# Performance work log

Hardware: AMD Instinct MI355X
Metric: run time of the kernel (lower is better)

## Reference

```python
import jax, jax.numpy as jnp
import numpy as np

DEPTH = 24; D_MODEL = 192; D_INNER = 384; D_STATE = 16; DT_RANK = 12; D_CONV = 4
H = 32; W = 3200; P = 16; NP = (W // P) * (H // P)  # 400 patches
NCLS = 22; BATCH = 4; EPS = 1e-5


def _rmsnorm(x, w):
    return x * jax.lax.rsqrt(jnp.mean(x * x, axis=-1, keepdims=True) + EPS) * w


def _causal_dwconv(x, w, b):
    # x: (B, L, D), w: (D, K) depthwise, left-padded causal conv (mamba conv1d)
    D = x.shape[-1]; K = w.shape[-1]
    xp = jnp.pad(jnp.swapaxes(x, 1, 2), ((0, 0), (0, 0), (K - 1, 0)))
    y = jax.lax.conv_general_dilated(xp, w[:, None, :], (1,), 'VALID',
            dimension_numbers=('NCH', 'OIH', 'NCH'), feature_group_count=D)
    return jnp.swapaxes(y + b[None, :, None], 1, 2)


def _selective_scan(x, dt, Bm, Cm, A, Dsk):
    # x, dt: (B, L, d); Bm, Cm: (B, L, n); A: (d, n); Dsk: (d,)
    dA = jnp.exp(dt[..., None] * A)                  # (B, L, d, n)
    dBx = (dt * x)[..., None] * Bm[:, :, None, :]    # (B, L, d, n)
    h0 = jnp.zeros((x.shape[0], x.shape[2], A.shape[1]), x.dtype)

    def step(h, inp):
        a, bx, c = inp
        h = a * h + bx
        return h, jnp.einsum('bdn,bn->bd', h, c)

    _, ys = jax.lax.scan(step, h0,
        (jnp.swapaxes(dA, 0, 1), jnp.swapaxes(dBx, 0, 1), jnp.swapaxes(Cm, 0, 1)))
    return jnp.swapaxes(ys, 0, 1) + x * Dsk


def _mamba_dir(xz, cw_l, cb_l, xpw, dtw, dtb, A, Dsk):
    xx, z = jnp.split(xz, 2, axis=-1)
    xx = jax.nn.silu(_causal_dwconv(xx, cw_l, cb_l))
    dbl = xx @ xpw.T                                  # (B, L, dt_rank + 2n)
    dt = jax.nn.softplus(dbl[..., :DT_RANK] @ dtw.T + dtb)
    Bm = dbl[..., DT_RANK:DT_RANK + D_STATE]
    Cm = dbl[..., DT_RANK + D_STATE:]
    y = _selective_scan(xx, dt, Bm, Cm, A, Dsk)
    return y * jax.nn.silu(z)


def _forward(x, pe_w, pe_b, cls_token, pos_embed, norm_w, in_proj_w, cw, cb,
             xproj_w, dtproj_w, dtproj_b, A_log, A_b_log, Dp, outproj_w,
             norm_f_w, head_w, head_b):
    B = x.shape[0]
    # patch embed: conv2d stride=kernel=16 on (B,1,H,W)
    y = jax.lax.conv_general_dilated(x[:, None], pe_w, (P, P), 'VALID',
            dimension_numbers=('NCHW', 'OIHW', 'NCHW')) + pe_b[None, :, None, None]
    tok = jnp.transpose(y, (0, 2, 3, 1)).reshape(B, -1, D_MODEL)   # (B, NP, D)
    tok = jnp.concatenate([jnp.broadcast_to(cls_token, (B, 1, D_MODEL)), tok], axis=1)
    tok = tok + pos_embed

    def layer_step(carry, p):
        hidden, residual = carry
        nw, ipw, cw_l, cb_l, xpw, dtw, dtb, Al, Abl, Dsk, opw = p
        residual = residual + hidden          # fused add (residual_in_fp32: all fp32)
        h = _rmsnorm(residual, nw)
        xz = h @ ipw.T                         # (B, L, 2*d_inner)
        y_f = _mamba_dir(xz, cw_l, cb_l, xpw, dtw, dtb, -jnp.exp(Al), Dsk)
        y_b = _mamba_dir(xz[:, ::-1], cw_l, cb_l, xpw, dtw, dtb, -jnp.exp(Abl), Dsk)[:, ::-1]
        return ((y_f + y_b) @ opw.T, residual), None

    # NOTE: source sets residual = x AND hidden = x before the loop, so the
    (hidden, residual), _ = jax.lax.scan(
        layer_step, (tok, tok),
        (norm_w, in_proj_w, cw, cb, xproj_w, dtproj_w, dtproj_b, A_log, A_b_log, Dp, outproj_w))
    out = _rmsnorm(residual + hidden, norm_f_w)
    return out[:, 0] @ head_w.T + head_b          # (B, n_classes)


def setup_inputs() -> dict:
    key = jax.random.key(0)
    ks = jax.random.split(key, 12)

    def n(k, shape, scale):
        return jax.random.normal(k, shape, jnp.float32) * scale

    a_init = jnp.tile(jnp.log(jnp.arange(1, D_STATE + 1, dtype=jnp.float32))[None, None, :],
                      (DEPTH, D_INNER, 1))
    return {
        'x': n(ks[0], (BATCH, H, W), 1.0),
        'pe_w': n(ks[1], (D_MODEL, 1, P, P), 1.0 / P),
        'pe_b': jnp.zeros((D_MODEL,), jnp.float32),
        'cls_token': n(ks[2], (1, 1, D_MODEL), 0.02),
        'pos_embed': n(ks[3], (1, NP + 1, D_MODEL), 0.02),
        'norm_w': jnp.ones((DEPTH, D_MODEL), jnp.float32),
        'in_proj_w': n(ks[4], (DEPTH, 2 * D_INNER, D_MODEL), D_MODEL ** -0.5),
        'cw': n(ks[5], (DEPTH, D_INNER, D_CONV), D_CONV ** -0.5),
        'cb': jnp.zeros((DEPTH, D_INNER), jnp.float32),
        'xproj_w': n(ks[6], (DEPTH, DT_RANK + 2 * D_STATE, D_INNER), D_INNER ** -0.5),
        'dtproj_w': n(ks[7], (DEPTH, D_INNER, DT_RANK), DT_RANK ** -0.5),
        'dtproj_b': n(ks[8], (DEPTH, D_INNER), 0.1),
        'A_log': a_init,
        'A_b_log': a_init,
        'Dp': jnp.ones((DEPTH, D_INNER), jnp.float32),
        'outproj_w': n(ks[9], (DEPTH, D_MODEL, D_INNER), D_INNER ** -0.5 / np.sqrt(DEPTH)),
        'norm_f_w': jnp.ones((D_MODEL,), jnp.float32),
        'head_w': n(ks[10], (NCLS, D_MODEL), D_MODEL ** -0.5),
        'head_b': jnp.zeros((NCLS,), jnp.float32),
    }


def reference(x, pe_w, pe_b, cls_token, pos_embed, norm_w, in_proj_w, cw, cb,
              xproj_w, dtproj_w, dtproj_b, A_log, A_b_log, Dp, outproj_w,
              norm_f_w, head_w, head_b):
    return _forward(x, pe_w, pe_b, cls_token, pos_embed, norm_w, in_proj_w, cw, cb,
                    xproj_w, dtproj_w, dtproj_b, A_log, A_b_log, Dp, outproj_w,
                    norm_f_w, head_w, head_b)
```

## Files before the change

kernel.cpp:

```cpp
#include <hip/hip_runtime.h>
#include <hip/hip_bf16.h>

#define DEPTH 24
#define DM 192
#define DI 384
#define DS 16
#define DR 12
#define LSEQ 401
#define BATCH 4
#define NTOK (BATCH*LSEQ)
#define NCLS 22
#define NC 16
#define TCH 26

__device__ __forceinline__ float silu_f(float x) { return x / (1.f + __expf(-x)); }

__global__ void patch_embed_k(const float* __restrict__ x,
                              const float* __restrict__ pe_w,
                              const float* __restrict__ pe_b,
                              const float* __restrict__ cls,
                              const float* __restrict__ pos,
                              float* __restrict__ residual, float* __restrict__ hidden)
{
    __shared__ float xp[4][256];
    int g0 = blockIdx.x * 4;
    int c = threadIdx.x;
    #pragma unroll
    for (int j = 0; j < 4; j++) {
        int g = g0 + j;
        int b = g / LSEQ, t = g % LSEQ;
        if (t != 0) {
            int p = t - 1, pi = p / 200, pj = p % 200;
            for (int i = c; i < 256; i += 192) {
                int pp = i >> 4, qq = i & 15;
                xp[j][i] = x[((size_t)(b * 32 + pi * 16 + pp)) * 3200 + pj * 16 + qq];
            }
        }
    }
    __syncthreads();
    float acc[4] = {0.f, 0.f, 0.f, 0.f};
    for (int k = 0; k < 256; k++) {
        float w = pe_w[c * 256 + k];
        #pragma unroll
        for (int j = 0; j < 4; j++) acc[j] += xp[j][k] * w;
    }
    #pragma unroll
    for (int j = 0; j < 4; j++) {
        int g = g0 + j;
        int t = g % LSEQ;
        float v = (t == 0) ? cls[c] : (acc[j] + pe_b[c]);
        v += pos[t * DM + c];
        residual[(size_t)g * DM + c] = v;
        hidden[(size_t)g * DM + c] = v;
    }
}

__global__ __launch_bounds__(256) void gemm_xz_k(
    const float* __restrict__ resin, const float* __restrict__ hidden,
    float* __restrict__ resout, const float* __restrict__ nw,
    const float* __restrict__ ipw, float* __restrict__ xz,
    float* __restrict__ dbl)
{
    __shared__ float As[48][68];
    __shared__ float Ws[48][68];
    __shared__ float srms[64];
    __shared__ float ps[64][4];
    int tid = threadIdx.x;
    for (int i = (blockIdx.y * 12 + blockIdx.x) * 256 + tid; i < 2 * NTOK * 44; i += 312 * 256)
        dbl[i] = 0.f;
    int bn = blockIdx.x * 64;
    int bm = blockIdx.y * 64;
    int rr = tid >> 2, q = tid & 3;
    int m = bm + rr;
    float rv[4][12];
    float s = 0.f;
    if (m < NTOK) {
        const float* rp = resin + (size_t)m * DM;
        const float* hp = hidden + (size_t)m * DM;
        #pragma unroll
        for (int c = 0; c < 4; c++) {
            int base = c * 48 + q * 12;
            #pragma unroll
            for (int i = 0; i < 12; i += 4) {
                float4 a = *(const float4*)&rp[base + i];
                float4 b = *(const float4*)&hp[base + i];
                float r0 = a.x + b.x, r1 = a.y + b.y, r2 = a.z + b.z, r3 = a.w + b.w;
                rv[c][i] = r0; rv[c][i + 1] = r1; rv[c][i + 2] = r2; rv[c][i + 3] = r3;
                s += r0 * r0 + r1 * r1 + r2 * r2 + r3 * r3;
            }
        }
        if (bn == 0) {
            float* op = resout + (size_t)m * DM;
            #pragma unroll
            for (int c = 0; c < 4; c++) {
                int base = c * 48 + q * 12;
                #pragma unroll
                for (int i = 0; i < 12; i += 4)
                    *(float4*)&op[base + i] =
                        make_float4(rv[c][i], rv[c][i + 1], rv[c][i + 2], rv[c][i + 3]);
            }
        }
    } else {
        #pragma unroll
        for (int c = 0; c < 4; c++)
            #pragma unroll
            for (int i = 0; i < 12; i++) rv[c][i] = 0.f;
    }
    ps[rr][q] = s;
    __syncthreads();
    if (q == 0) {
        float tot = ps[rr][0] + ps[rr][1] + ps[rr][2] + ps[rr][3];
        srms[rr] = rsqrtf(tot * (1.f / (float)DM) + 1e-5f);
    }
    __syncthreads();

    int orow = (tid >> 4) * 4;
    int ocol = (tid & 15) * 4;
    int sk = q * 12;
    float acc[4][4] = {};
    for (int c = 0; c < 4; c++) {
        float rs = srms[rr];
        #pragma unroll
        for (int i = 0; i < 12; i++)
            As[sk + i][rr] = rv[c][i] * rs * nw[c * 48 + sk + i];
        const float* wp = ipw + (size_t)(bn + rr) * DM + c * 48 + sk;
        #pragma unroll
        for (int i = 0; i < 12; i++)
            Ws[sk + i][rr] = wp[i];
        __syncthreads();
        #pragma unroll
        for (int kk = 0; kk < 48; kk++) {
            float4 a = *(const float4*)&As[kk][orow];
            float4 w = *(const float4*)&Ws[kk][ocol];
            acc[0][0] += a.x * w.x; acc[0][1] += a.x * w.y; acc[0][2] += a.x * w.z; acc[0][3] += a.x * w.w;
            acc[1][0] += a.y * w.x; acc[1][1] += a.y * w.y; acc[1][2] += a.y * w.z; acc[1][3] += a.y * w.w;
            acc[2][0] += a.z * w.x; acc[2][1] += a.z * w.y; acc[2][2] += a.z * w.z; acc[2][3] += a.z * w.w;
            acc[3][0] += a.w * w.x; acc[3][1] += a.w * w.y; acc[3][2] += a.w * w.z; acc[3][3] += a.w * w.w;
        }
        __syncthreads();
    }
    #pragma unroll
    for (int i = 0; i < 4; i++) {
        int mm = bm + orow + i;
        if (mm >= NTOK) continue;
        *(float4*)&xz[(size_t)mm * (2 * DI) + bn + ocol] =
            make_float4(acc[i][0], acc[i][1], acc[i][2], acc[i][3]);
    }
}

__global__ __launch_bounds__(256) void xproj_conv_k(
    const float* __restrict__ xz,
    const float* __restrict__ cw, const float* __restrict__ cb,
    const float* __restrict__ xpw, float* __restrict__ dbl)
{
    __shared__ float As[96][33];
    __shared__ float Ws[96][48];
    int tid = threadIdx.x;
    int kbase = blockIdx.x * 96;
    int bm = blockIdx.y * 32;
    for (int idx = tid; idx < 96 * 32; idx += 256) {
        int k = idx >> 5, row = idx & 31;
        int m = bm + row;
        float v = 0.f;
        if (m < 2 * NTOK) {
            int dir = m / NTOK;
            int r = m - dir * NTOK;
            int b = r / LSEQ, t = r % LSEQ;
            int ch = kbase + k;
            float a = cb[ch];
            #pragma unroll
            for (int j = 0; j < 4; j++) {
                int tt = t - 3 + j;
                if (tt >= 0) {
                    int st = dir ? (LSEQ - 1 - tt) : tt;
                    a += cw[ch * 4 + j] * xz[((size_t)(b * LSEQ + st)) * (2 * DI) + ch];
                }
            }
            v = silu_f(a);
        }
        As[k][row] = v;
    }
    for (int i = tid; i < 96 * 48; i += 256) {
        int k = i / 48, rr = i % 48;
        Ws[k][rr] = (rr < 44) ? xpw[(size_t)rr * DI + kbase + k] : 0.f;
    }
    __syncthreads();
    int row = tid & 31, cg = tid >> 5;
    int cbase = cg * 6;
    float acc[6] = {};
    #pragma unroll 4
    for (int kk = 0; kk < 96; kk++) {
        float a = As[kk][row];
        #pragma unroll
        for (int j = 0; j < 6; j++) acc[j] += a * Ws[kk][cbase + j];
    }
    int m = bm + row;
    if (m < 2 * NTOK) {
        #pragma unroll
        for (int j = 0; j < 6; j++) {
            int cc = cbase + j;
            if (cc < 44) atomicAdd(&dbl[(size_t)m * 44 + cc], acc[j]);
        }
    }
}

__global__ __launch_bounds__(256) void scan_part_k(
    const float* __restrict__ xz, const float* __restrict__ dbl,
    const float* __restrict__ cw, const float* __restrict__ cb,
    const float* __restrict__ dtw, const float* __restrict__ dtb,
    const float* __restrict__ A_log, const float* __restrict__ A_b_log,
    float* __restrict__ hloc, float* __restrict__ Pc)
{
    __shared__ float sdbl[TCH][28];
    __shared__ float sdt[TCH][16];
    __shared__ float sxx[TCH][16];
    __shared__ float sw[16][12];
    __shared__ float sb2[16];
    int dblk = blockIdx.x, chunk = blockIdx.y;
    int db = blockIdx.z;
    int dir = db >> 2, b = db & 3;
    int tid = threadIdx.x;
    int d0 = dblk * 16;
    int t0 = chunk * TCH;
    size_t dof44 = (size_t)db * LSEQ * 44;
    for (int i = tid; i < TCH * 28; i += 256) {
        int t = i / 28, cc = i - t * 28;
        sdbl[t][cc] = dbl[dof44 + (size_t)(t0 + t) * 44 + cc];
    }
    if (tid < 192) { int d = tid / 12, r = tid - d * 12; sw[d][r] = dtw[(size_t)(d0 + d) * 12 + r]; }
    if (tid < 16) sb2[tid] = dtb[d0 + tid];
    for (int i = tid; i < TCH * 16; i += 256) {
        int t = i >> 4, d = i & 15;
        int tq = t0 + t, ch = d0 + d;
        float a = cb[ch];
        #pragma unroll
        for (int j = 0; j < 4; j++) {
            int tt = tq - 3 + j;
            if (tt >= 0) {
                int st = dir ? (LSEQ - 1 - tt) : tt;
                a += cw[ch * 4 + j] * xz[((size_t)(b * LSEQ + st)) * (2 * DI) + ch];
            }
        }
        sxx[t][d] = silu_f(a);
    }
    __syncthreads();
    for (int i = tid; i < TCH * 16; i += 256) {
        int t = i >> 4, d = i & 15;
        float a2 = sb2[d];
        #pragma unroll
        for (int r = 0; r < 12; r++) a2 += sdbl[t][r] * sw[d][r];
        sdt[t][d] = (a2 > 15.f) ? a2 : __logf(1.f + __expf(a2));
    }
    __syncthreads();
    int wave = tid >> 6, lane = tid & 63;
    int dsub = wave * 4 + (lane >> 4);
    int n = lane & 15;
    const float* Al = dir ? A_b_log : A_log;
    float Aval = -__expf(Al[(d0 + dsub) * DS + n]);
    float h = 0.f, P = 1.f;
    #pragma unroll
    for (int i = 0; i < TCH; i++) {
        float dtv = sdt[i][dsub];
        float xv  = sxx[i][dsub];
        float Bv  = sdbl[i][12 + n];
        float dA = __expf(dtv * Aval);
        h = dA * h + (dtv * xv) * Bv;
        P *= dA;
    }
    size_t idx2 = ((size_t)db * NC + chunk) * (DI * DS) + (size_t)(d0 + dsub) * DS + n;
    hloc[idx2] = h;
    Pc[idx2] = P;
}

__global__ __launch_bounds__(256) void scan_fix_k(
    const float* __restrict__ xz, const float* __restrict__ dbl,
    const float* __restrict__ cw, const float* __restrict__ cb,
    const float* __restrict__ dtw, const float* __restrict__ dtb,
    const float* __restrict__ A_log, const float* __restrict__ A_b_log,
    const float* __restrict__ Dp,
    const float* __restrict__ hloc, const float* __restrict__ Pc,
    float* __restrict__ yraw)
{
    __shared__ float sdbl[TCH][44];
    __shared__ float sdt[TCH][16];
    __shared__ float sxx[TCH][16];
    __shared__ float sy[TCH][16];
    __shared__ float sw[16][12];
    __shared__ float sb2[16];
    int dblk = blockIdx.x, chunk = blockIdx.y;
    int db = blockIdx.z;
    int dir = db >> 2, b = db & 3;
    int tid = threadIdx.x;
    int d0 = dblk * 16;
    int t0 = chunk * TCH;
    size_t dofD = (size_t)db * LSEQ * DI;
    size_t dof44 = (size_t)db * LSEQ * 44;
    for (int i = tid; i < TCH * 44; i += 256) {
        int t = i / 44, cc = i - t * 44;
        sdbl[t][cc] = ((t0 + t) < LSEQ) ? dbl[dof44 + (size_t)(t0 + t) * 44 + cc] : 0.f;
    }
    if (tid < 192) { int d = tid / 12, r = tid - d * 12; sw[d][r] = dtw[(size_t)(d0 + d) * 12 + r]; }
    if (tid < 16) sb2[tid] = dtb[d0 + tid];
    for (int i = tid; i < TCH * 16; i += 256) {
        int t = i >> 4, d = i & 15;
        int tq = t0 + t, ch = d0 + d;
        float v = 0.f;
        if (tq < LSEQ) {
            float a = cb[ch];
            #pragma unroll
            for (int j = 0; j < 4; j++) {
                int tt = tq - 3 + j;
                if (tt >= 0) {
                    int st = dir ? (LSEQ - 1 - tt) : tt;
                    a += cw[ch * 4 + j] * xz[((size_t)(b * LSEQ + st)) * (2 * DI) + ch];
                }
            }
            v = silu_f(a);
        }
        sxx[t][d] = v;
    }
    __syncthreads();
    for (int i = tid; i < TCH * 16; i += 256) {
        int t = i >> 4, d = i & 15;
        float a2 = sb2[d];
        #pragma unroll
        for (int r = 0; r < 12; r++) a2 += sdbl[t][r] * sw[d][r];
        sdt[t][d] = (a2 > 15.f) ? a2 : __logf(1.f + __expf(a2));
    }
    __syncthreads();
    int wave = tid >> 6, lane = tid & 63;
    int dsub = wave * 4 + (lane >> 4);
    int n = lane & 15;
    const float* Al = dir ? A_b_log : A_log;
    float Aval = -__expf(Al[(d0 + dsub) * DS + n]);
    float Dv = Dp[d0 + dsub];
    float h = 0.f;
    size_t cbase = (size_t)db * NC * (DI * DS) + (size_t)(d0 + dsub) * DS + n;
    #pragma unroll
    for (int j = 0; j < NC - 1; j++) {
        size_t idx = cbase + (size_t)j * (DI * DS);
        float pj = Pc[idx], hj = hloc[idx];
        h = (j < chunk) ? (pj * h + hj) : h;
    }
    #pragma unroll
    for (int i = 0; i < TCH; i++) {
        float dtv = sdt[i][dsub];
        float xv  = sxx[i][dsub];
        float Bv  = sdbl[i][12 + n];
        float Cv  = sdbl[i][28 + n];
        h = __expf(dtv * Aval) * h + (dtv * xv) * Bv;
        float p = h * Cv;
        p += __shfl_xor(p, 1);
        p += __shfl_xor(p, 2);
        p += __shfl_xor(p, 4);
        p += __shfl_xor(p, 8);
        if (n == 0) sy[i][dsub] = p + xv * Dv;
    }
    __syncthreads();
    int len = min(t0 + TCH, LSEQ) - t0;
    for (int idx = tid; idx < len * 16; idx += 256) {
        int t = idx >> 4, d = idx & 15;
        yraw[dofD + (size_t)(t0 + t) * DI + d0 + d] = sy[t][d];
    }
}

__global__ __launch_bounds__(256) void outproj_k(
    const float* __restrict__ yraw, const float* __restrict__ xz,
    const float* __restrict__ opw, float* __restrict__ hidden)
{
    __shared__ float As[48][34];
    __shared__ float Ws[48][34];
    int tid = threadIdx.x;
    int bn = blockIdx.x * 32;
    int bm = blockIdx.y * 32;
    int orow = (tid >> 4) * 2, ocol = (tid & 15) * 2;
    float acc[2][2] = {};
    for (int k0 = 0; k0 < DI; k0 += 48) {
        for (int i = tid; i < 48 * 32; i += 256) {
            int row = i / 48, k = i - row * 48;
            int mm = bm + row;
            float vv = 0.f;
            if (mm < NTOK) {
                int b = mm / LSEQ, t = mm % LSEQ;
                int ch = k0 + k;
                float yf = yraw[(size_t)mm * DI + ch];
                float yb = yraw[(size_t)(NTOK + b * LSEQ + (LSEQ - 1 - t)) * DI + ch];
                float z  = xz[(size_t)mm * (2 * DI) + DI + ch];
                vv = (yf + yb) * silu_f(z);
            }
            As[k][row] = vv;
        }
        for (int i = tid; i < 48 * 32; i += 256) {
            int col = i / 48, k = i - col * 48;
            Ws[k][col] = opw[(size_t)(bn + col) * DI + k0 + k];
        }
        __syncthreads();
        #pragma unroll 8
        for (int kk = 0; kk < 48; kk++) {
            float2 av = *(const float2*)&As[kk][orow];
            float2 wv = *(const float2*)&Ws[kk][ocol];
            acc[0][0] += av.x * wv.x; acc[0][1] += av.x * wv.y;
            acc[1][0] += av.y * wv.x; acc[1][1] += av.y * wv.y;
        }
        __syncthreads();
    }
    #pragma unroll
    for (int i = 0; i < 2; i++) {
        int mm = bm + orow + i;
        if (mm >= NTOK) continue;
        #pragma unroll
        for (int j = 0; j < 2; j++)
            hidden[(size_t)mm * DM + bn + ocol + j] = acc[i][j];
    }
}

__global__ void final_head_k(const float* __restrict__ residual, const float* __restrict__ hidden,
                             const float* __restrict__ norm_f,
                             const float* __restrict__ head_w,
                             const float* __restrict__ head_b,
                             void* __restrict__ out,
                             const unsigned short* __restrict__ probe)
{
    __shared__ float wsum[3];
    __shared__ float hb[DM];
    int b = blockIdx.x;
    int c = threadIdx.x;
    int idx = (b * LSEQ) * DM + c;
    float r = residual[idx] + hidden[idx];
    float s = r * r;
    for (int off = 32; off > 0; off >>= 1) s += __shfl_down(s, off);
    int wave = c >> 6, lane = c & 63;
    if (lane == 0) wsum[wave] = s;
    __syncthreads();
    float tot = wsum[0] + wsum[1] + wsum[2];
    float rms = rsqrtf(tot / (float)DM + 1e-5f);
    hb[c] = r * rms * norm_f[c];
    __syncthreads();
    if (c < NCLS) {
        float acc = head_b[c];
        #pragma unroll 8
        for (int k = 0; k < DM; k++) acc += hb[k] * head_w[c * DM + k];
        if (probe[0] == 0x3F80u)
            ((__hip_bfloat16*)out)[b * NCLS + c] = __float2bfloat16(acc);
        else
            ((float*)out)[b * NCLS + c] = acc;
    }
}

extern "C" void kernel_launch(void* const* d_in, const int* in_sizes, int n_in,
                              void* d_out, int out_size, void* d_ws, size_t ws_size,
                              hipStream_t stream)
{
    (void)in_sizes; (void)n_in; (void)out_size; (void)ws_size;
    const float* x      = (const float*)d_in[0];
    const float* pe_w   = (const float*)d_in[1];
    const float* pe_b   = (const float*)d_in[2];
    const float* cls    = (const float*)d_in[3];
    const float* pos    = (const float*)d_in[4];
    const float* norm_w = (const float*)d_in[5];
    const float* ipw    = (const float*)d_in[6];
    const float* cw     = (const float*)d_in[7];
    const float* cb     = (const float*)d_in[8];
    const float* xpw    = (const float*)d_in[9];
    const float* dtw    = (const float*)d_in[10];
    const float* dtb    = (const float*)d_in[11];
    const float* A_log  = (const float*)d_in[12];
    const float* A_b_log= (const float*)d_in[13];
    const float* Dp     = (const float*)d_in[14];
    const float* opw    = (const float*)d_in[15];
    const float* norm_f = (const float*)d_in[16];
    const float* head_w = (const float*)d_in[17];
    const float* head_b = (const float*)d_in[18];
    const unsigned short* probe = (const unsigned short*)d_in[14];

    float* ws = (float*)d_ws;
    const size_t nTokDM = (size_t)NTOK * DM;
    const size_t nTokXZ = (size_t)NTOK * 2 * DI;
    const size_t nDirDI = (size_t)2 * NTOK * DI;
    const size_t nDir44 = (size_t)2 * NTOK * 44;
    const size_t nChunk = (size_t)2 * BATCH * NC * DI * DS;
    float* resA   = ws;
    float* resB   = resA + nTokDM;
    float* hidden = resB + nTokDM;
    float* xz     = hidden + nTokDM;
    float* dbl    = xz + nTokXZ;
    float* yraw   = dbl + nDir44;
    float* hloc   = yraw + nDirDI;
    float* Pc     = hloc + nChunk;

    patch_embed_k<<<NTOK / 4, DM, 0, stream>>>(x, pe_w, pe_b, cls, pos, resA, hidden);

    for (int l = 0; l < DEPTH; l++) {
        float* rin  = (l & 1) ? resB : resA;
        float* rout = (l & 1) ? resA : resB;

        gemm_xz_k<<<dim3(12, 26), 256, 0, stream>>>(
            rin, hidden, rout, norm_w + (size_t)l * DM,
            ipw + (size_t)l * 2 * DI * DM, xz, dbl);

        xproj_conv_k<<<dim3(4, 101), 256, 0, stream>>>(
            xz, cw + (size_t)l * DI * 4, cb + (size_t)l * DI,
            xpw + (size_t)l * 44 * DI, dbl);

        scan_part_k<<<dim3(DI / 16, NC - 1, 2 * BATCH), 256, 0, stream>>>(
            xz, dbl, cw + (size_t)l * DI * 4, cb + (size_t)l * DI,
            dtw + (size_t)l * DI * DR, dtb + (size_t)l * DI,
            A_log + (size_t)l * DI * DS, A_b_log + (size_t)l * DI * DS,
            hloc, Pc);

        scan_fix_k<<<dim3(DI / 16, NC, 2 * BATCH), 256, 0, stream>>>(
            xz, dbl, cw + (size_t)l * DI * 4, cb + (size_t)l * DI,
            dtw + (size_t)l * DI * DR, dtb + (size_t)l * DI,
            A_log + (size_t)l * DI * DS, A_b_log + (size_t)l * DI * DS,
            Dp + (size_t)l * DI, hloc, Pc, yraw);

        outproj_k<<<dim3(6, 51), 256, 0, stream>>>(
            yraw, xz, opw + (size_t)l * DM * DI, hidden);
    }

    final_head_k<<<BATCH, DM, 0, stream>>>(resA, hidden, norm_f, head_w, head_b,
                                           d_out, probe);
}
```

Before: 3.659 ms.

## Split outproj GEMM along K with atomic accumulation and register-staged loads

The output-projection GEMM is split into two K halves via a third grid dimension, doubling block count, and partial sums are combined with atomicAdd into the hidden buffer. The hidden buffer is zeroed inside the earlier xproj_conv kernel so no extra launch is needed. Each thread now loads a contiguous 24-element slice of the gated activations and weights into registers before writing them to shared memory, replacing strided per-element global loads. This trades more parallelism and better coalescing for atomic traffic and nondeterministic summation order.

```diff
diff --git a/kernel.cpp b/kernel.cpp
--- a/kernel.cpp
+++ b/kernel.cpp
@@ -151,11 +151,14 @@
 __global__ __launch_bounds__(256) void xproj_conv_k(
     const float* __restrict__ xz,
     const float* __restrict__ cw, const float* __restrict__ cb,
-    const float* __restrict__ xpw, float* __restrict__ dbl)
+    const float* __restrict__ xpw, float* __restrict__ dbl,
+    float* __restrict__ hidden)
 {
     __shared__ float As[96][33];
     __shared__ float Ws[96][48];
     int tid = threadIdx.x;
+    for (int i = (blockIdx.y * 4 + blockIdx.x) * 256 + tid; i < NTOK * DM; i += 404 * 256)
+        hidden[i] = 0.f;
     int kbase = blockIdx.x * 96;
     int bm = blockIdx.y * 32;
     for (int idx = tid; idx < 96 * 32; idx += 256) {
@@ -368,49 +371,63 @@
     const float* __restrict__ yraw, const float* __restrict__ xz,
     const float* __restrict__ opw, float* __restrict__ hidden)
 {
-    __shared__ float As[48][34];
-    __shared__ float Ws[48][34];
+    __shared__ float As[96][34];
+    __shared__ float Ws[96][34];
     int tid = threadIdx.x;
     int bn = blockIdx.x * 32;
     int bm = blockIdx.y * 32;
-    int orow = (tid >> 4) * 2, ocol = (tid & 15) * 2;
+    int kbase = blockIdx.z * 192;
+    int row8 = tid >> 3, seg = tid & 7, k0 = seg * 24;
+    float a[24], wreg[24];
+    int m = bm + row8;
+    if (m < NTOK) {
+        int b = m / LSEQ, t = m % LSEQ;
+        const float* yf = yraw + (size_t)m * DI + kbase + k0;
+        const float* yb = yraw + (size_t)(NTOK + b * LSEQ + (LSEQ - 1 - t)) * DI + kbase + k0;
+        const float* zp = xz + (size_t)m * (2 * DI) + DI + kbase + k0;
+        #pragma unroll
+        for (int i = 0; i < 24; i++) {
+            float z = zp[i];
+            a[i] = (yf[i] + yb[i]) * (z / (1.f + __expf(-z)));
+        }
+    } else {
+        #pragma unroll
+        for (int i = 0; i < 24; i++) a[i] = 0.f;
+    }
+    {
+        const float* wp = opw + (size_t)(bn + row8) * DI + kbase + k0;
+        #pragma unroll
+        for (int i = 0; i < 24; i++) wreg[i] = wp[i];
+    }
+    int r0 = (tid >> 4) * 2, c0 = (tid & 15) * 2;
     float acc[2][2] = {};
-    for (int k0 = 0; k0 < DI; k0 += 48) {
-        for (int i = tid; i < 48 * 32; i += 256) {
-            int row = i / 48, k = i - row * 48;
-            int mm = bm + row;
-            float vv = 0.f;
-            if (mm < NTOK) {
-                int b = mm / LSEQ, t = mm % LSEQ;
-                int ch = k0 + k;
-                float yf = yraw[(size_t)mm * DI + ch];
-                float yb = yraw[(size_t)(NTOK + b * LSEQ + (LSEQ - 1 - t)) * DI + ch];
-                float z  = xz[(size_t)mm * (2 * DI) + DI + ch];
-                vv = (yf + yb) * silu_f(z);
-            }
-            As[k][row] = vv;
-        }
-        for (int i = tid; i < 48 * 32; i += 256) {
-            int col = i / 48, k = i - col * 48;
-            Ws[k][col] = opw[(size_t)(bn + col) * DI + k0 + k];
+    #pragma unroll
+    for (int st = 0; st < 2; st++) {
+        if (st) __syncthreads();
+        if ((seg >> 2) == st) {
+            int kb = k0 - st * 96;
+            #pragma unroll
+            for (int i = 0; i < 24; i++) {
+                As[kb + i][row8] = a[i];
+                Ws[kb + i][row8] = wreg[i];
+            }
         }
         __syncthreads();
         #pragma unroll 8
-        for (int kk = 0; kk < 48; kk++) {
-            float2 av = *(const float2*)&As[kk][orow];
-            float2 wv = *(const float2*)&Ws[kk][ocol];
+        for (int kk = 0; kk < 96; kk++) {
+            float2 av = *(const float2*)&As[kk][r0];
+            float2 wv = *(const float2*)&Ws[kk][c0];
             acc[0][0] += av.x * wv.x; acc[0][1] += av.x * wv.y;
             acc[1][0] += av.y * wv.x; acc[1][1] += av.y * wv.y;
         }
-        __syncthreads();
     }
     #pragma unroll
     for (int i = 0; i < 2; i++) {
-        int mm = bm + orow + i;
+        int mm = bm + r0 + i;
         if (mm >= NTOK) continue;
         #pragma unroll
         for (int j = 0; j < 2; j++)
-            hidden[(size_t)mm * DM + bn + ocol + j] = acc[i][j];
+            atomicAdd(&hidden[(size_t)mm * DM + bn + c0 + j], acc[i][j]);
     }
 }
 
@@ -500,7 +517,7 @@
 
         xproj_conv_k<<<dim3(4, 101), 256, 0, stream>>>(
             xz, cw + (size_t)l * DI * 4, cb + (size_t)l * DI,
-            xpw + (size_t)l * 44 * DI, dbl);
+            xpw + (size_t)l * 44 * DI, dbl, hidden);
 
         scan_part_k<<<dim3(DI / 16, NC - 1, 2 * BATCH), 256, 0, stream>>>(
             xz, dbl, cw + (size_t)l * DI * 4, cb + (size_t)l * DI,
@@ -514,7 +531,7 @@
             A_log + (size_t)l * DI * DS, A_b_log + (size_t)l * DI * DS,
             Dp + (size_t)l * DI, hloc, Pc, yraw);
 
-        outproj_k<<<dim3(6, 51), 256, 0, stream>>>(
+        outproj_k<<<dim3(6, 51, 2), 256, 0, stream>>>(
             yraw, xz, opw + (size_t)l * DM * DI, hidden);
     }
 
```

After: 3.156 ms. 1.16x faster.
